# Optimization experiments

Hardware: AMD Instinct MI355X
Metric: run time of the kernel (lower is better)

The kernel has to match this reference:

```python
import jax, jax.numpy as jnp
import numpy as np

B, F, E = 1024, 1024, 256      # batch, flat_shape (mobilenet), embedding_size
L1, L2, L3 = 16, 8, 32         # level1 classes, level2 classes per branch, level3 classes per leaf
NE3 = L1 * L2                  # 128 leaf (level-3) classifier heads


def setup_inputs() -> dict:
    key = jax.random.key(0)
    ks = jax.random.split(key, 10)
    w = lambda k, shape: (jax.random.normal(k, shape, jnp.float32) * 0.02)
    return {
        "features_x": jax.random.normal(ks[0], (B, F), jnp.float32),
        "features_y": jax.random.normal(ks[1], (B, F), jnp.float32),
        # level-1 head: Linear(F->E, no bias) + LayerNorm + ReLU + Linear(E->L1)
        "l1_W1": w(ks[2], (F, E)),
        "l1_g": jnp.ones((E,), jnp.float32), "l1_b": jnp.zeros((E,), jnp.float32),
        "l1_W2": w(ks[3], (E, L1)), "l1_b2": jnp.zeros((L1,), jnp.float32),
        # level-2 heads (one per level-1 class), stacked on a leading expert axis
        "l2_W1": w(ks[4], (L1, F, E)),
        "l2_g": jnp.ones((L1, E), jnp.float32), "l2_b": jnp.zeros((L1, E), jnp.float32),
        "l2_W2": w(ks[5], (L1, E, L2)), "l2_b2": jnp.zeros((L1, L2), jnp.float32),
        # level-3 heads (flattened [level1][level2] -> NE3 experts)
        "l3_W1": w(ks[6], (NE3, F, E)),
        "l3_g": jnp.ones((NE3, E), jnp.float32), "l3_b": jnp.zeros((NE3, E), jnp.float32),
        "l3_W2": w(ks[7], (NE3, E, L3)), "l3_b2": jnp.zeros((NE3, L3), jnp.float32),
    }


def _ln(h, g, b, eps=1e-5):
    m = jnp.mean(h, axis=-1, keepdims=True)
    v = jnp.mean(jnp.square(h - m), axis=-1, keepdims=True)
    return (h - m) * jax.lax.rsqrt(v + eps) * g + b


def reference(features_x, features_y,
              l1_W1, l1_g, l1_b, l1_W2, l1_b2,
              l2_W1, l2_g, l2_b, l2_W2, l2_b2,
              l3_W1, l3_g, l3_b, l3_W2, l3_b2):
    # Dropout is identity in eval mode.
    x, y = features_x, features_y
    rows = jnp.arange(x.shape[0])

    # level 1: single head on x
    h1 = jax.nn.relu(_ln(x @ l1_W1, l1_g, l1_b))
    logits1 = h1 @ l1_W2 + l1_b2                                # [B, L1]
    idx1 = jnp.argmax(logits1, axis=-1)                         # argmax(softmax) == argmax

    # level 2: routed head on 0.6*x + 0.4*y; compute all L1 heads batched, gather selected
    ft = 0.6 * x + 0.4 * y
    h2 = jax.nn.relu(_ln(jnp.einsum('bf,efh->beh', ft, l2_W1), l2_g, l2_b))  # [B, L1, E]
    logits2_all = jnp.einsum('beh,ehc->bec', h2, l2_W2) + l2_b2              # [B, L1, L2]
    logits2 = logits2_all[rows, idx1]                                        # [B, L2]
    idx2 = jnp.argmax(logits2, axis=-1)

    # level 3: doubly-routed head on x; flat expert index = idx1*L2 + idx2
    eidx = idx1 * logits2.shape[-1] + idx2
    h3 = jax.nn.relu(_ln(jnp.einsum('bf,efh->beh', x, l3_W1), l3_g, l3_b))   # [B, NE3, E]
    logits3_all = jnp.einsum('beh,ehc->bec', h3, l3_W2) + l3_b2              # [B, NE3, L3]
    logits3 = logits3_all[rows, eidx]                                        # [B, L3]

    # uniform class counts => pad_sequence is a no-op
    return (logits1, logits2, logits3)
```

## Files before the change

kernel.cpp:

```cpp
#include <hip/hip_runtime.h>


#define B_    1024
#define F_    1024
#define E_    256
#define NL1   16
#define NL2   8
#define NL3   32
#define NE3_  128
#define CS1   2
#define CS2   4
#define CS3   16
#define KS3   4
#define MAXCH2 272
#define MAXCH3 192
#define OUT2_OFF (B_ * NL1)
#define OUT3_OFF (B_ * (NL1 + NL2))
#define H4_BYTE_OFF 65536
#define H4_BYTES   ((size_t)MAXCH3 * KS3 * 16 * E_ * 4)
#define HNS (E_ + 4)

typedef __attribute__((ext_vector_type(8))) short bf16x8_t;
typedef __attribute__((ext_vector_type(4))) float f32x4_t;

__device__ __forceinline__ float b2f(unsigned short u) {
    union { unsigned int i; float f; } v; v.i = ((unsigned int)u) << 16; return v.f;
}
__device__ __forceinline__ unsigned short f2b(float f) {
    union { float f; unsigned int i; } v; v.f = f;
    unsigned int x = v.i; x += 0x7fffu + ((x >> 16) & 1u);
    return (unsigned short)(x >> 16);
}

template<int R, int NC>
__device__ void head_chunk(
    const float* __restrict__ in,
    const void* W1v, const void* gv_, const void* bv_,
    const void* W2v, const void* b2v, int bf,
    float* part, float* hn, float* red, float* lg, int t)
{
    const int lane = t & 63;
    const int grp  = t >> 6;
    const int e0   = lane * 4;

    float acc[R][4];
    #pragma unroll
    for (int r = 0; r < R; ++r) { acc[r][0]=0.f; acc[r][1]=0.f; acc[r][2]=0.f; acc[r][3]=0.f; }

    const float* ing = in + grp * 256;

    if (bf) {
        const unsigned short* W = (const unsigned short*)W1v + (size_t)grp * 256 * E_;
        for (int f0 = 0; f0 < 256; f0 += 16) {
            ushort4 w[16];
            #pragma unroll
            for (int k = 0; k < 16; ++k)
                w[k] = *(const ushort4*)(W + (size_t)(f0 + k) * E_ + e0);
            #pragma unroll
            for (int q = 0; q < 4; ++q) {
                float4 xq[R];
                #pragma unroll
                for (int r = 0; r < R; ++r)
                    xq[r] = *(const float4*)(ing + r * F_ + f0 + q * 4);
                #pragma unroll
                for (int k2 = 0; k2 < 4; ++k2) {
                    ushort4 ww = w[q * 4 + k2];
                    float w0 = b2f(ww.x), w1 = b2f(ww.y), w2 = b2f(ww.z), w3 = b2f(ww.w);
                    #pragma unroll
                    for (int r = 0; r < R; ++r) {
                        float xv = (k2 == 0) ? xq[r].x : (k2 == 1) ? xq[r].y
                                 : (k2 == 2) ? xq[r].z : xq[r].w;
                        acc[r][0] += xv * w0; acc[r][1] += xv * w1;
                        acc[r][2] += xv * w2; acc[r][3] += xv * w3;
                    }
                }
            }
        }
    } else {
        const float* W = (const float*)W1v + (size_t)grp * 256 * E_;
        for (int f0 = 0; f0 < 256; f0 += 8) {
            float4 w[8];
            #pragma unroll
            for (int k = 0; k < 8; ++k)
                w[k] = *(const float4*)(W + (size_t)(f0 + k) * E_ + e0);
            #pragma unroll
            for (int q = 0; q < 2; ++q) {
                float4 xq[R];
                #pragma unroll
                for (int r = 0; r < R; ++r)
                    xq[r] = *(const float4*)(ing + r * F_ + f0 + q * 4);
                #pragma unroll
                for (int k2 = 0; k2 < 4; ++k2) {
                    float4 ww = w[q * 4 + k2];
                    #pragma unroll
                    for (int r = 0; r < R; ++r) {
                        float xv = (k2 == 0) ? xq[r].x : (k2 == 1) ? xq[r].y
                                 : (k2 == 2) ? xq[r].z : xq[r].w;
                        acc[r][0] += xv * ww.x; acc[r][1] += xv * ww.y;
                        acc[r][2] += xv * ww.z; acc[r][3] += xv * ww.w;
                    }
                }
            }
        }
    }

    #pragma unroll
    for (int r = 0; r < R; ++r) {
        part[(size_t)(grp * R + r) * E_ + e0 + 0] = acc[r][0];
        part[(size_t)(grp * R + r) * E_ + e0 + 1] = acc[r][1];
        part[(size_t)(grp * R + r) * E_ + e0 + 2] = acc[r][2];
        part[(size_t)(grp * R + r) * E_ + e0 + 3] = acc[r][3];
    }
    __syncthreads();

    float h[R];
    #pragma unroll
    for (int r = 0; r < R; ++r)
        h[r] = part[(0 * R + r) * E_ + t] + part[(1 * R + r) * E_ + t]
             + part[(2 * R + r) * E_ + t] + part[(3 * R + r) * E_ + t];

    #pragma unroll
    for (int r = 0; r < R; ++r) {
        float s = h[r], ss = h[r] * h[r];
        #pragma unroll
        for (int o = 32; o > 0; o >>= 1) { s += __shfl_xor(s, o); ss += __shfl_xor(ss, o); }
        if (lane == 0) { red[(grp * R + r) * 2 + 0] = s; red[(grp * R + r) * 2 + 1] = ss; }
    }
    __syncthreads();

    float gv, bv;
    if (bf) { gv = b2f(((const unsigned short*)gv_)[t]); bv = b2f(((const unsigned short*)bv_)[t]); }
    else    { gv = ((const float*)gv_)[t];               bv = ((const float*)bv_)[t]; }

    #pragma unroll
    for (int r = 0; r < R; ++r) {
        float S  = red[(0*R+r)*2] + red[(1*R+r)*2] + red[(2*R+r)*2] + red[(3*R+r)*2];
        float SS = red[(0*R+r)*2+1] + red[(1*R+r)*2+1] + red[(2*R+r)*2+1] + red[(3*R+r)*2+1];
        float m    = S * (1.0f / E_);
        float var  = SS * (1.0f / E_) - m * m;
        float rstd = rsqrtf(var + 1e-5f);
        hn[r * HNS + t] = fmaxf((h[r] - m) * rstd * gv + bv, 0.0f);
    }
    __syncthreads();

    constexpr int RN = R * NC;
    constexpr int G  = 4;
    constexpr int CH = E_ / G;
    float a = 0.f;
    if (t < RN * G) {
        const int oi = t % RN, j = t / RN, r = oi / NC, c = oi % NC;
        if (bf) {
            const unsigned short* W = (const unsigned short*)W2v;
            #pragma unroll 8
            for (int e = j * CH; e < j * CH + CH; ++e) a += hn[r * HNS + e] * b2f(W[(size_t)e * NC + c]);
        } else {
            const float* W = (const float*)W2v;
            #pragma unroll 8
            for (int e = j * CH; e < j * CH + CH; ++e) a += hn[r * HNS + e] * W[(size_t)e * NC + c];
        }
    }
    part[t] = a;
    __syncthreads();
    if (t < RN) {
        const int c = t % NC;
        float sum = part[t] + part[RN + t] + part[2 * RN + t] + part[3 * RN + t];
        float bias = bf ? b2f(((const unsigned short*)b2v)[c]) : ((const float*)b2v)[c];
        lg[t] = sum + bias;
    }
    __syncthreads();
}

__global__ void dtype_sniff_kernel(const unsigned int* l1g_words, int* flag) {
    if (threadIdx.x == 0 && blockIdx.x == 0)
        *flag = (l1g_words[0] == 0x3F803F80u) ? 1 : 0;
}

__global__ __launch_bounds__(256) void mlc_level1_kernel(
    const void* x, const void* W1, const void* g, const void* b,
    const void* W2, const void* b2, void* out, int* idx1, const int* flagp)
{
    __shared__ float in_s[CS1 * F_];
    __shared__ float part[4 * CS1 * E_];
    __shared__ float hn[CS1 * HNS];
    __shared__ float red[4 * CS1 * 2];
    __shared__ float lg[CS1 * NL1];

    const int t = threadIdx.x;
    const int bf = *flagp;
    const int row0 = blockIdx.x * CS1;

    #pragma unroll
    for (int r = 0; r < CS1; ++r) {
        if (bf) {
            ushort4 xv = ((const ushort4*)x)[(size_t)(row0 + r) * 256 + t];
            in_s[r * F_ + t*4+0] = b2f(xv.x); in_s[r * F_ + t*4+1] = b2f(xv.y);
            in_s[r * F_ + t*4+2] = b2f(xv.z); in_s[r * F_ + t*4+3] = b2f(xv.w);
        } else {
            float4 xv = ((const float4*)x)[(size_t)(row0 + r) * 256 + t];
            in_s[r * F_ + t*4+0] = xv.x; in_s[r * F_ + t*4+1] = xv.y;
            in_s[r * F_ + t*4+2] = xv.z; in_s[r * F_ + t*4+3] = xv.w;
        }
    }
    __syncthreads();

    head_chunk<CS1, NL1>(in_s, W1, g, b, W2, b2, bf, part, hn, red, lg, t);

    if (t < CS1 * NL1) {
        int r = t / NL1, c = t % NL1;
        size_t o = (size_t)(row0 + r) * NL1 + c;
        if (bf) ((unsigned short*)out)[o] = f2b(lg[t]);
        else    ((float*)out)[o] = lg[t];
        if (c == 0) {
            float best = lg[r * NL1]; int bi = 0;
            #pragma unroll
            for (int cc = 1; cc < NL1; ++cc)
                if (lg[r * NL1 + cc] > best) { best = lg[r * NL1 + cc]; bi = cc; }
            idx1[row0 + r] = bi;
        }
    }
}

template<int NEXP, int MAXCH, int CHUNK>
__global__ __launch_bounds__(1024) void mlc_route_kernel(
    const int* __restrict__ src, int* __restrict__ rows_out, int4* __restrict__ chunks_out)
{
    __shared__ int hist[NEXP], offs[NEXP], cur[NEXP], cOff[NEXP];
    __shared__ int sA[NEXP], sB[NEXP];
    const int t = threadIdx.x;
    if (t < NEXP) hist[t] = 0;
    __syncthreads();
    int e = src[t];
    if (e < 0) e = 0; if (e >= NEXP) e = NEXP - 1;
    atomicAdd(&hist[e], 1);
    __syncthreads();
    if (t < NEXP) { sA[t] = hist[t]; sB[t] = (hist[t] + CHUNK - 1) / CHUNK; }
    __syncthreads();
    for (int d = 1; d < NEXP; d <<= 1) {
        int va = 0, vb = 0;
        if (t < NEXP && t >= d) { va = sA[t - d]; vb = sB[t - d]; }
        __syncthreads();
        if (t < NEXP) { sA[t] += va; sB[t] += vb; }
        __syncthreads();
    }
    if (t < NEXP) {
        int ex = sA[t] - hist[t];
        offs[t] = ex; cur[t] = ex;
        cOff[t] = sB[t] - (hist[t] + CHUNK - 1) / CHUNK;
    }
    __syncthreads();
    int pos = atomicAdd(&cur[e], 1);
    if (pos >= 0 && pos < B_) rows_out[pos] = t;
    const int ctot = sB[NEXP - 1];
    if (t < NEXP) {
        int n = hist[t], st = offs[t], c0 = cOff[t], k = 0;
        for (int j = 0; j < n; j += CHUNK, ++k)
            chunks_out[c0 + k] = make_int4(t, st + j, min(CHUNK, n - j), 0);
    }
    for (int s = ctot + t; s < MAXCH; s += 1024) chunks_out[s] = make_int4(0, 0, 0, 0);
}

__global__ __launch_bounds__(256) void mlc_level2_kernel(
    const void* x, const void* y,
    const void* W1b, const void* gb, const void* bb,
    const void* W2b, const void* b2b,
    const int4* __restrict__ chunks, const int* __restrict__ rowlist,
    void* out, int* eidx, const int* flagp)
{
    __shared__ float in_s[CS2 * F_];
    __shared__ float part[4 * CS2 * E_];
    __shared__ float hn[CS2 * HNS];
    __shared__ float red[4 * CS2 * 2];
    __shared__ float lg[CS2 * NL2];
    __shared__ int4  chs;
    __shared__ int   rows_s[CS2];

    const int t = threadIdx.x;
    const int bf = *flagp;

    if (t == 0) chs = chunks[blockIdx.x];
    __syncthreads();
    const int expert = chs.x, start = chs.y, count = chs.z;
    if (count <= 0) return;
    if (t < CS2) rows_s[t] = (t < count) ? rowlist[start + t] : -1;
    __syncthreads();

    #pragma unroll
    for (int r = 0; r < CS2; ++r) {
        int row = rows_s[r];
        float f0 = 0.f, f1 = 0.f, f2 = 0.f, f3 = 0.f;
        if (row >= 0) {
            if (bf) {
                ushort4 xv = ((const ushort4*)x)[(size_t)row * 256 + t];
                ushort4 yv = ((const ushort4*)y)[(size_t)row * 256 + t];
                f0 = 0.6f * b2f(xv.x) + 0.4f * b2f(yv.x);
                f1 = 0.6f * b2f(xv.y) + 0.4f * b2f(yv.y);
                f2 = 0.6f * b2f(xv.z) + 0.4f * b2f(yv.z);
                f3 = 0.6f * b2f(xv.w) + 0.4f * b2f(yv.w);
            } else {
                float4 xv = ((const float4*)x)[(size_t)row * 256 + t];
                float4 yv = ((const float4*)y)[(size_t)row * 256 + t];
                f0 = 0.6f * xv.x + 0.4f * yv.x; f1 = 0.6f * xv.y + 0.4f * yv.y;
                f2 = 0.6f * xv.z + 0.4f * yv.z; f3 = 0.6f * xv.w + 0.4f * yv.w;
            }
        }
        in_s[r * F_ + t*4+0] = f0; in_s[r * F_ + t*4+1] = f1;
        in_s[r * F_ + t*4+2] = f2; in_s[r * F_ + t*4+3] = f3;
    }
    __syncthreads();

    const void* W1 = bf ? (const void*)((const unsigned short*)W1b + (size_t)expert * F_ * E_)
                        : (const void*)((const float*)W1b + (size_t)expert * F_ * E_);
    const void* g  = bf ? (const void*)((const unsigned short*)gb + (size_t)expert * E_)
                        : (const void*)((const float*)gb + (size_t)expert * E_);
    const void* b  = bf ? (const void*)((const unsigned short*)bb + (size_t)expert * E_)
                        : (const void*)((const float*)bb + (size_t)expert * E_);
    const void* W2 = bf ? (const void*)((const unsigned short*)W2b + (size_t)expert * E_ * NL2)
                        : (const void*)((const float*)W2b + (size_t)expert * E_ * NL2);
    const void* b2 = bf ? (const void*)((const unsigned short*)b2b + (size_t)expert * NL2)
                        : (const void*)((const float*)b2b + (size_t)expert * NL2);

    head_chunk<CS2, NL2>(in_s, W1, g, b, W2, b2, bf, part, hn, red, lg, t);

    if (t < CS2 * NL2) {
        int r = t / NL2, c = t % NL2;
        if (r < count) {
            size_t o = (size_t)OUT2_OFF + (size_t)rows_s[r] * NL2 + c;
            if (bf) ((unsigned short*)out)[o] = f2b(lg[t]);
            else    ((float*)out)[o] = lg[t];
            if (c == 0) {
                float best = lg[r * NL2]; int bi = 0;
                #pragma unroll
                for (int cc = 1; cc < NL2; ++cc)
                    if (lg[r * NL2 + cc] > best) { best = lg[r * NL2 + cc]; bi = cc; }
                eidx[rows_s[r]] = expert * NL2 + bi;
            }
        }
    }
}


__global__ __launch_bounds__(256) void mlc_l3_partial_kernel(
    const void* x, const void* W1b,
    const int4* __restrict__ chunks, const int* __restrict__ rowlist,
    float* __restrict__ h4, const int* flagp)
{
    __shared__ __align__(16) unsigned short xs[16 * 256];
    __shared__ int4 chs;
    __shared__ int  rows_s[16];

    const int t  = threadIdx.x;
    const int bf = *flagp;
    const int c  = blockIdx.x >> 2;
    const int ks = blockIdx.x & 3;

    if (t == 0) chs = chunks[c];
    __syncthreads();
    const int expert = chs.x, start = chs.y, count = chs.z;
    if (count <= 0) return;
    if (t < 16) rows_s[t] = (t < count) ? rowlist[start + t] : -1;
    __syncthreads();

    {
        const int r = t >> 4;
        const int row = rows_s[r];
        #pragma unroll
        for (int i = 0; i < 2; ++i) {
            const int c2 = (t & 15) + 16 * i;
            const int cs = c2 ^ (r & 7);
            uint4 v = make_uint4(0u, 0u, 0u, 0u);
            if (row >= 0) {
                if (bf) {
                    v = *(const uint4*)((const unsigned short*)x + (size_t)row * F_ + ks * 256 + c2 * 8);
                } else {
                    const float* xf = (const float*)x + (size_t)row * F_ + ks * 256 + c2 * 8;
                    float4 fa = *(const float4*)xf;
                    float4 fb = *(const float4*)(xf + 4);
                    v.x = ((unsigned)f2b(fa.y) << 16) | f2b(fa.x);
                    v.y = ((unsigned)f2b(fa.w) << 16) | f2b(fa.z);
                    v.z = ((unsigned)f2b(fb.y) << 16) | f2b(fb.x);
                    v.w = ((unsigned)f2b(fb.w) << 16) | f2b(fb.z);
                }
            }
            *(uint4*)(xs + r * 256 + cs * 8) = v;
        }
    }
    __syncthreads();

    const int l    = t & 63;
    const int w    = t >> 6;
    const int u    = l >> 4;
    const int row  = l & 15;
    const int colb = w * 64 + row;

    f32x4_t acc[4];
    #pragma unroll
    for (int tl = 0; tl < 4; ++tl) acc[tl] = (f32x4_t){0.f, 0.f, 0.f, 0.f};

    if (bf) {
        const unsigned short* __restrict__ W =
            (const unsigned short*)W1b + (size_t)expert * F_ * E_ + (size_t)ks * 256 * E_;
        #pragma unroll 2
        for (int k0 = 0; k0 < 256; k0 += 32) {
            const int cs = ((k0 >> 3) + u) ^ (row & 7);
            bf16x8_t ax = *(const bf16x8_t*)(xs + row * 256 + cs * 8);
            const unsigned short* __restrict__ Wk = W + (size_t)(k0 + u * 8) * E_ + colb;
            #pragma unroll
            for (int tl = 0; tl < 4; ++tl) {
                bf16x8_t b;
                #pragma unroll
                for (int e = 0; e < 8; ++e) b[e] = (short)Wk[e * E_ + tl * 16];
                acc[tl] = __builtin_amdgcn_mfma_f32_16x16x32_bf16(ax, b, acc[tl], 0, 0, 0);
            }
        }
    } else {
        const float* __restrict__ W =
            (const float*)W1b + (size_t)expert * F_ * E_ + (size_t)ks * 256 * E_;
        #pragma unroll 2
        for (int k0 = 0; k0 < 256; k0 += 32) {
            const int cs = ((k0 >> 3) + u) ^ (row & 7);
            bf16x8_t ax = *(const bf16x8_t*)(xs + row * 256 + cs * 8);
            const float* __restrict__ Wk = W + (size_t)(k0 + u * 8) * E_ + colb;
            #pragma unroll
            for (int tl = 0; tl < 4; ++tl) {
                bf16x8_t b;
                #pragma unroll
                for (int e = 0; e < 8; ++e) b[e] = (short)f2b(Wk[e * E_ + tl * 16]);
                acc[tl] = __builtin_amdgcn_mfma_f32_16x16x32_bf16(ax, b, acc[tl], 0, 0, 0);
            }
        }
    }

    float* hd = h4 + (size_t)(c * KS3 + ks) * 16 * E_;
    #pragma unroll
    for (int tl = 0; tl < 4; ++tl) {
        #pragma unroll
        for (int j = 0; j < 4; ++j)
            hd[(size_t)(u * 4 + j) * E_ + colb + tl * 16] = acc[tl][j];
    }
}

__global__ __launch_bounds__(256) void MultiLevelClassifier_26491358282059_kernel(
    const void* gb, const void* bb, const void* W2b, const void* b2b,
    const int4* __restrict__ chunks, const int* __restrict__ rowlist,
    const float* __restrict__ h4, void* out, const int* flagp)
{
    __shared__ float hn[8 * HNS];
    __shared__ float red[4 * 8 * 2];
    __shared__ int4  chs;
    __shared__ int   rows_s[16];

    const int t    = threadIdx.x;
    const int bf   = *flagp;
    const int c    = blockIdx.x >> 1;
    const int half = blockIdx.x & 1;

    if (t == 0) chs = chunks[c];
    __syncthreads();
    const int expert = chs.x, start = chs.y, count = chs.z;
    if (count <= 0) return;
    if (t < 16) rows_s[t] = (t < count) ? rowlist[start + t] : -1;
    __syncthreads();

    const int l = t & 63, w = t >> 6;

    float hv[8];
    #pragma unroll
    for (int m = 0; m < 8; ++m) {
        const float* p = h4 + (size_t)(c * KS3) * 16 * E_ + (size_t)(half * 8 + m) * E_ + t;
        hv[m] = p[0] + p[16 * E_] + p[32 * E_] + p[48 * E_];
    }

    #pragma unroll
    for (int m = 0; m < 8; ++m) {
        float s = hv[m], ss = hv[m] * hv[m];
        #pragma unroll
        for (int o = 32; o > 0; o >>= 1) { s += __shfl_xor(s, o); ss += __shfl_xor(ss, o); }
        if (l == 0) { red[(w * 8 + m) * 2] = s; red[(w * 8 + m) * 2 + 1] = ss; }
    }
    __syncthreads();

    float gv, bv;
    if (bf) {
        gv = b2f(((const unsigned short*)gb)[(size_t)expert * E_ + t]);
        bv = b2f(((const unsigned short*)bb)[(size_t)expert * E_ + t]);
    } else {
        gv = ((const float*)gb)[(size_t)expert * E_ + t];
        bv = ((const float*)bb)[(size_t)expert * E_ + t];
    }

    #pragma unroll
    for (int m = 0; m < 8; ++m) {
        float S  = red[m * 2]     + red[(8 + m) * 2]     + red[(16 + m) * 2]     + red[(24 + m) * 2];
        float SS = red[m * 2 + 1] + red[(8 + m) * 2 + 1] + red[(16 + m) * 2 + 1] + red[(24 + m) * 2 + 1];
        float mean = S * (1.0f / E_);
        float var  = SS * (1.0f / E_) - mean * mean;
        float rstd = rsqrtf(var + 1e-5f);
        hn[m * HNS + t] = fmaxf((hv[m] - mean) * rstd * gv + bv, 0.0f);
    }
    __syncthreads();

    {
        const int r = t >> 5, c0 = t & 31;
        float a = 0.f;
        if (bf) {
            const unsigned short* W = (const unsigned short*)W2b + (size_t)expert * E_ * NL3;
            #pragma unroll 8
            for (int e = 0; e < E_; ++e) a += hn[r * HNS + e] * b2f(W[(size_t)e * NL3 + c0]);
        } else {
            const float* W = (const float*)W2b + (size_t)expert * E_ * NL3;
            #pragma unroll 8
            for (int e = 0; e < E_; ++e) a += hn[r * HNS + e] * W[(size_t)e * NL3 + c0];
        }
        const int rr = half * 8 + r;
        if (rr < count) {
            float bias = bf ? b2f(((const unsigned short*)b2b)[(size_t)expert * NL3 + c0])
                            : ((const float*)b2b)[(size_t)expert * NL3 + c0];
            size_t o = (size_t)OUT3_OFF + (size_t)rows_s[rr] * NL3 + c0;
            if (bf) ((unsigned short*)out)[o] = f2b(a + bias);
            else    ((float*)out)[o] = a + bias;
        }
    }
}

__device__ __forceinline__ void stage_rows_full(
    unsigned short* xs, const void* xg, const int* rows, int bf, int t)
{
    const int r = t >> 4;
    const int row = rows[r];
    #pragma unroll
    for (int i = 0; i < 8; ++i) {
        const int c  = (t & 15) + 16 * i;
        const int cs = c ^ (r & 7);
        uint4 v = make_uint4(0u, 0u, 0u, 0u);
        if (row >= 0) {
            if (bf) {
                v = *(const uint4*)((const unsigned short*)xg + (size_t)row * F_ + c * 8);
            } else {
                const float* xf = (const float*)xg + (size_t)row * F_ + c * 8;
                float4 fa = *(const float4*)xf;
                float4 fb = *(const float4*)(xf + 4);
                v.x = ((unsigned)f2b(fa.y) << 16) | f2b(fa.x);
                v.y = ((unsigned)f2b(fa.w) << 16) | f2b(fa.z);
                v.z = ((unsigned)f2b(fb.y) << 16) | f2b(fb.x);
                v.w = ((unsigned)f2b(fb.w) << 16) | f2b(fb.z);
            }
        }
        *(uint4*)(xs + (size_t)r * F_ + cs * 8) = v;
    }
}

__global__ __launch_bounds__(256) void mlc_level3_mono_kernel(
    const void* x,
    const void* W1b, const void* gb, const void* bb,
    const void* W2b, const void* b2b,
    const int4* __restrict__ chunks, const int* __restrict__ rowlist,
    void* out, const int* flagp)
{
    __shared__ __align__(16) unsigned short xs[16 * F_];
    __shared__ float h[16 * E_];
    __shared__ float red[128];
    __shared__ int4  chs;
    __shared__ int   rows_s[16];

    const int t  = threadIdx.x;
    const int bf = *flagp;

    if (t == 0) chs = chunks[blockIdx.x];
    __syncthreads();
    const int expert = chs.x, start = chs.y, count = chs.z;
    if (count <= 0) return;
    if (t < 16) rows_s[t] = (t < count) ? rowlist[start + t] : -1;
    __syncthreads();

    stage_rows_full(xs, x, rows_s, bf, t);
    __syncthreads();

    const int l = t & 63, w = t >> 6, u = l >> 4, row = l & 15;
    const int colb = w * 64 + row;
    f32x4_t acc[4];
    #pragma unroll
    for (int tl = 0; tl < 4; ++tl) acc[tl] = (f32x4_t){0.f, 0.f, 0.f, 0.f};

    if (bf) {
        const unsigned short* __restrict__ W = (const unsigned short*)W1b + (size_t)expert * F_ * E_;
        for (int k0 = 0; k0 < F_; k0 += 32) {
            const int cs = ((k0 >> 3) + u) ^ (row & 7);
            bf16x8_t ax = *(const bf16x8_t*)(xs + (size_t)row * F_ + cs * 8);
            const unsigned short* __restrict__ Wk = W + (size_t)(k0 + u * 8) * E_ + colb;
            #pragma unroll
            for (int tl = 0; tl < 4; ++tl) {
                bf16x8_t b;
                #pragma unroll
                for (int e = 0; e < 8; ++e) b[e] = (short)Wk[e * E_ + tl * 16];
                acc[tl] = __builtin_amdgcn_mfma_f32_16x16x32_bf16(ax, b, acc[tl], 0, 0, 0);
            }
        }
    } else {
        const float* __restrict__ W = (const float*)W1b + (size_t)expert * F_ * E_;
        for (int k0 = 0; k0 < F_; k0 += 32) {
            const int cs = ((k0 >> 3) + u) ^ (row & 7);
            bf16x8_t ax = *(const bf16x8_t*)(xs + (size_t)row * F_ + cs * 8);
            const float* __restrict__ Wk = W + (size_t)(k0 + u * 8) * E_ + colb;
            #pragma unroll
            for (int tl = 0; tl < 4; ++tl) {
                bf16x8_t b;
                #pragma unroll
                for (int e = 0; e < 8; ++e) b[e] = (short)f2b(Wk[e * E_ + tl * 16]);
                acc[tl] = __builtin_amdgcn_mfma_f32_16x16x32_bf16(ax, b, acc[tl], 0, 0, 0);
            }
        }
    }
    #pragma unroll
    for (int tl = 0; tl < 4; ++tl) {
        #pragma unroll
        for (int j = 0; j < 4; ++j)
            h[(size_t)(u * 4 + j) * E_ + colb + tl * 16] = acc[tl][j];
    }
    __syncthreads();

    float hv[16];
    #pragma unroll
    for (int r = 0; r < 16; ++r) hv[r] = h[(size_t)r * E_ + t];
    #pragma unroll
    for (int r = 0; r < 16; ++r) {
        float s = hv[r], ss = hv[r] * hv[r];
        #pragma unroll
        for (int o = 32; o > 0; o >>= 1) { s += __shfl_xor(s, o); ss += __shfl_xor(ss, o); }
        if (l == 0) { red[(w * 16 + r) * 2] = s; red[(w * 16 + r) * 2 + 1] = ss; }
    }
    __syncthreads();
    float gv, bv;
    if (bf) { gv = b2f(((const unsigned short*)gb)[(size_t)expert * E_ + t]);
              bv = b2f(((const unsigned short*)bb)[(size_t)expert * E_ + t]); }
    else    { gv = ((const float*)gb)[(size_t)expert * E_ + t];
              bv = ((const float*)bb)[(size_t)expert * E_ + t]; }
    #pragma unroll
    for (int r = 0; r < 16; ++r) {
        float S  = red[r * 2]     + red[(16 + r) * 2]     + red[(32 + r) * 2]     + red[(48 + r) * 2];
        float SS = red[r * 2 + 1] + red[(16 + r) * 2 + 1] + red[(32 + r) * 2 + 1] + red[(48 + r) * 2 + 1];
        float mean = S * (1.0f / E_);
        float var  = SS * (1.0f / E_) - mean * mean;
        float rstd = rsqrtf(var + 1e-5f);
        h[(size_t)r * E_ + t] = fmaxf((hv[r] - mean) * rstd * gv + bv, 0.0f);
    }
    __syncthreads();

    {
        const int r = t >> 4, c0 = t & 15;
        float a0 = 0.f, a1 = 0.f;
        if (bf) {
            const unsigned short* W = (const unsigned short*)W2b + (size_t)expert * E_ * NL3;
            #pragma unroll 4
            for (int e = 0; e < E_; ++e) {
                float hh = h[(size_t)r * E_ + e];
                a0 += hh * b2f(W[(size_t)e * NL3 + c0]);
                a1 += hh * b2f(W[(size_t)e * NL3 + c0 + 16]);
            }
        } else {
            const float* W = (const float*)W2b + (size_t)expert * E_ * NL3;
            #pragma unroll 4
            for (int e = 0; e < E_; ++e) {
                float hh = h[(size_t)r * E_ + e];
                a0 += hh * W[(size_t)e * NL3 + c0];
                a1 += hh * W[(size_t)e * NL3 + c0 + 16];
            }
        }
        if (r < count) {
            float bb0, bb1;
            if (bf) { bb0 = b2f(((const unsigned short*)b2b)[(size_t)expert * NL3 + c0]);
                      bb1 = b2f(((const unsigned short*)b2b)[(size_t)expert * NL3 + c0 + 16]); }
            else    { bb0 = ((const float*)b2b)[(size_t)expert * NL3 + c0];
                      bb1 = ((const float*)b2b)[(size_t)expert * NL3 + c0 + 16]; }
            size_t o = (size_t)OUT3_OFF + (size_t)rows_s[r] * NL3 + c0;
            if (bf) {
                ((unsigned short*)out)[o]      = f2b(a0 + bb0);
                ((unsigned short*)out)[o + 16] = f2b(a1 + bb1);
            } else {
                ((float*)out)[o]      = a0 + bb0;
                ((float*)out)[o + 16] = a1 + bb1;
            }
        }
    }
}

extern "C" void kernel_launch(void* const* d_in, const int* in_sizes, int n_in,
                              void* d_out, int out_size, void* d_ws, size_t ws_size,
                              hipStream_t stream) {
    (void)in_sizes; (void)n_in; (void)out_size;

    int* ws = (int*)d_ws;
    int*  flag  = ws;
    int*  idx1  = ws + 64;
    int*  eidx  = ws + 1088;
    int*  rows2 = ws + 2112;
    int*  rows3 = ws + 3136;
    int4* ch2   = (int4*)(ws + 4160);
    int4* ch3   = (int4*)(ws + 5248);
    float* h4   = (float*)((char*)d_ws + H4_BYTE_OFF);

    const bool big_ws = ws_size >= (size_t)H4_BYTE_OFF + H4_BYTES;

    dtype_sniff_kernel<<<1, 1, 0, stream>>>((const unsigned int*)d_in[3], flag);

    mlc_level1_kernel<<<B_ / CS1, 256, 0, stream>>>(
        d_in[0], d_in[2], d_in[3], d_in[4], d_in[5], d_in[6],
        d_out, idx1, flag);

    mlc_route_kernel<NL1, MAXCH2, CS2><<<1, 1024, 0, stream>>>(idx1, rows2, ch2);

    mlc_level2_kernel<<<MAXCH2, 256, 0, stream>>>(
        d_in[0], d_in[1], d_in[7], d_in[8], d_in[9], d_in[10], d_in[11],
        ch2, rows2, d_out, eidx, flag);

    mlc_route_kernel<NE3_, MAXCH3, CS3><<<1, 1024, 0, stream>>>(eidx, rows3, ch3);

    if (big_ws) {
        mlc_l3_partial_kernel<<<MAXCH3 * KS3, 256, 0, stream>>>(
            d_in[0], d_in[12], ch3, rows3, h4, flag);
        MultiLevelClassifier_26491358282059_kernel<<<MAXCH3 * 2, 256, 0, stream>>>(
            d_in[13], d_in[14], d_in[15], d_in[16],
            ch3, rows3, h4, d_out, flag);
    } else {
        mlc_level3_mono_kernel<<<MAXCH3, 256, 0, stream>>>(
            d_in[0], d_in[12], d_in[13], d_in[14], d_in[15], d_in[16],
            ch3, rows3, d_out, flag);
    }
}
```

Before: 329.1 us.

## Move level-1 and level-2 heads to split-K bf16 MFMA with near-tie fp32 cleanup

After: 516.5 us. 57.0% more time.

```diff
diff --git a/kernel.cpp b/kernel.cpp
--- a/kernel.cpp
+++ b/kernel.cpp
@@ -8,17 +8,18 @@
 #define NL2   8
 #define NL3   32
 #define NE3_  128
-#define CS1   2
-#define CS2   4
-#define CS3   16
-#define KS3   4
-#define MAXCH2 272
+#define NCH1  64
+#define MAXCH2 80
 #define MAXCH3 192
 #define OUT2_OFF (B_ * NL1)
 #define OUT3_OFF (B_ * (NL1 + NL2))
 #define H4_BYTE_OFF 65536
-#define H4_BYTES   ((size_t)MAXCH3 * KS3 * 16 * E_ * 4)
+#define H4_BYTES   ((size_t)MAXCH3 * 4 * 16 * E_ * 4)
 #define HNS (E_ + 4)
+#define MARGIN 4.0e-3f
+#define CS1F  2
+#define CS2F  4
+#define MAXCH2F 272
 
 typedef __attribute__((ext_vector_type(8))) short bf16x8_t;
 typedef __attribute__((ext_vector_type(4))) float f32x4_t;
@@ -170,27 +171,581 @@
     __syncthreads();
 }
 
-__global__ void dtype_sniff_kernel(const unsigned int* l1g_words, int* flag) {
-    if (threadIdx.x == 0 && blockIdx.x == 0)
+__global__ void dtype_sniff_kernel(const unsigned int* l1g_words, int* flag,
+                                   int* fcnt1, int* fcnt2) {
+    if (threadIdx.x == 0 && blockIdx.x == 0) {
         *flag = (l1g_words[0] == 0x3F803F80u) ? 1 : 0;
-}
-
-__global__ __launch_bounds__(256) void mlc_level1_kernel(
+        *fcnt1 = 0; *fcnt2 = 0;
+    }
+}
+
+template<int DUAL>
+__device__ __forceinline__ void mfma_slice(
+    const unsigned short* xs, const unsigned short* ys,
+    const void* Wv, int bf, f32x4_t accx[4], f32x4_t accy[4], int t)
+{
+    const int l = t & 63, w = t >> 6, u = l >> 4, row = l & 15;
+    const int colb = w * 64 + row;
+    if (bf) {
+        const unsigned short* __restrict__ W = (const unsigned short*)Wv;
+        #pragma unroll 2
+        for (int k0 = 0; k0 < 256; k0 += 32) {
+            const int cs = ((k0 >> 3) + u) ^ (row & 7);
+            bf16x8_t ax = *(const bf16x8_t*)(xs + row * 256 + cs * 8);
+            bf16x8_t ay{};
+            if (DUAL) ay = *(const bf16x8_t*)(ys + row * 256 + cs * 8);
+            const unsigned short* __restrict__ Wk = W + (size_t)(k0 + u * 8) * E_ + colb;
+            #pragma unroll
+            for (int tl = 0; tl < 4; ++tl) {
+                bf16x8_t b;
+                #pragma unroll
+                for (int e = 0; e < 8; ++e) b[e] = (short)Wk[e * E_ + tl * 16];
+                accx[tl] = __builtin_amdgcn_mfma_f32_16x16x32_bf16(ax, b, accx[tl], 0, 0, 0);
+                if (DUAL)
+                    accy[tl] = __builtin_amdgcn_mfma_f32_16x16x32_bf16(ay, b, accy[tl], 0, 0, 0);
+            }
+        }
+    } else {
+        const float* __restrict__ W = (const float*)Wv;
+        #pragma unroll 2
+        for (int k0 = 0; k0 < 256; k0 += 32) {
+            const int cs = ((k0 >> 3) + u) ^ (row & 7);
+            bf16x8_t ax = *(const bf16x8_t*)(xs + row * 256 + cs * 8);
+            bf16x8_t ay{};
+            if (DUAL) ay = *(const bf16x8_t*)(ys + row * 256 + cs * 8);
+            const float* __restrict__ Wk = W + (size_t)(k0 + u * 8) * E_ + colb;
+            #pragma unroll
+            for (int tl = 0; tl < 4; ++tl) {
+                bf16x8_t b;
+                #pragma unroll
+                for (int e = 0; e < 8; ++e) b[e] = (short)f2b(Wk[e * E_ + tl * 16]);
+                accx[tl] = __builtin_amdgcn_mfma_f32_16x16x32_bf16(ax, b, accx[tl], 0, 0, 0);
+                if (DUAL)
+                    accy[tl] = __builtin_amdgcn_mfma_f32_16x16x32_bf16(ay, b, accy[tl], 0, 0, 0);
+            }
+        }
+    }
+}
+
+__device__ __forceinline__ void stage_slice_row(
+    unsigned short* xs, const void* xg, int row, int ks, int bf, int t)
+{
+    const int r = t >> 4;
+    #pragma unroll
+    for (int i = 0; i < 2; ++i) {
+        const int c2 = (t & 15) + 16 * i;
+        const int cs = c2 ^ (r & 7);
+        uint4 v = make_uint4(0u, 0u, 0u, 0u);
+        if (row >= 0) {
+            if (bf) {
+                v = *(const uint4*)((const unsigned short*)xg + (size_t)row * F_ + ks * 256 + c2 * 8);
+            } else {
+                const float* xf = (const float*)xg + (size_t)row * F_ + ks * 256 + c2 * 8;
+                float4 fa = *(const float4*)xf;
+                float4 fb = *(const float4*)(xf + 4);
+                v.x = ((unsigned)f2b(fa.y) << 16) | f2b(fa.x);
+                v.y = ((unsigned)f2b(fa.w) << 16) | f2b(fa.z);
+                v.z = ((unsigned)f2b(fb.y) << 16) | f2b(fb.x);
+                v.w = ((unsigned)f2b(fb.w) << 16) | f2b(fb.z);
+            }
+        }
+        *(uint4*)(xs + r * 256 + cs * 8) = v;
+    }
+}
+
+__device__ __forceinline__ void write_slice(float* hd, const f32x4_t acc[4], int t) {
+    const int l = t & 63, w = t >> 6, u = l >> 4, row = l & 15;
+    const int colb = w * 64 + row;
+    #pragma unroll
+    for (int tl = 0; tl < 4; ++tl) {
+        #pragma unroll
+        for (int j = 0; j < 4; ++j)
+            hd[(size_t)(u * 4 + j) * E_ + colb + tl * 16] = acc[tl][j];
+    }
+}
+
+__global__ __launch_bounds__(256) void mlc_l1_partial_kernel(
+    const void* x, const void* W1, float* __restrict__ h4, const int* flagp)
+{
+    __shared__ __align__(16) unsigned short xs[16 * 256];
+    const int t = threadIdx.x, bf = *flagp;
+    const int c = blockIdx.x >> 2, ks = blockIdx.x & 3;
+    stage_slice_row(xs, x, c * 16 + (t >> 4), ks, bf, t);
+    __syncthreads();
+    f32x4_t acc[4];
+    #pragma unroll
+    for (int tl = 0; tl < 4; ++tl) acc[tl] = (f32x4_t){0.f, 0.f, 0.f, 0.f};
+    const void* Ws = bf ? (const void*)((const unsigned short*)W1 + (size_t)ks * 256 * E_)
+                        : (const void*)((const float*)W1 + (size_t)ks * 256 * E_);
+    mfma_slice<0>(xs, nullptr, Ws, bf, acc, nullptr, t);
+    write_slice(h4 + (size_t)(c * 4 + ks) * 16 * E_, acc, t);
+}
+
+__global__ __launch_bounds__(256) void mlc_l1_final_kernel(
+    const void* g, const void* b, const void* W2, const void* b2,
+    const float* __restrict__ h4, void* out, int* idx1,
+    int* fcnt, int* flist, const int* flagp)
+{
+    __shared__ float hn[8 * HNS];
+    __shared__ float red[64];
+    __shared__ float lgs[8 * NL1];
+    const int t = threadIdx.x, bf = *flagp;
+    const int c = blockIdx.x >> 1, half = blockIdx.x & 1;
+    const int l = t & 63, w = t >> 6;
+
+    float hv[8];
+    #pragma unroll
+    for (int m = 0; m < 8; ++m) {
+        const float* p = h4 + (size_t)(c * 4) * 16 * E_ + (size_t)(half * 8 + m) * E_ + t;
+        hv[m] = p[0] + p[16 * E_] + p[32 * E_] + p[48 * E_];
+    }
+    #pragma unroll
+    for (int m = 0; m < 8; ++m) {
+        float s = hv[m], ss = hv[m] * hv[m];
+        #pragma unroll
+        for (int o = 32; o > 0; o >>= 1) { s += __shfl_xor(s, o); ss += __shfl_xor(ss, o); }
+        if (l == 0) { red[(w * 8 + m) * 2] = s; red[(w * 8 + m) * 2 + 1] = ss; }
+    }
+    __syncthreads();
+    float gv, bv;
+    if (bf) { gv = b2f(((const unsigned short*)g)[t]); bv = b2f(((const unsigned short*)b)[t]); }
+    else    { gv = ((const float*)g)[t];               bv = ((const float*)b)[t]; }
+    #pragma unroll
+    for (int m = 0; m < 8; ++m) {
+        float S  = red[m * 2]     + red[(8 + m) * 2]     + red[(16 + m) * 2]     + red[(24 + m) * 2];
+        float SS = red[m * 2 + 1] + red[(8 + m) * 2 + 1] + red[(16 + m) * 2 + 1] + red[(24 + m) * 2 + 1];
+        float mean = S * (1.0f / E_);
+        float var  = SS * (1.0f / E_) - mean * mean;
+        float rstd = rsqrtf(var + 1e-5f);
+        hn[m * HNS + t] = fmaxf((hv[m] - mean) * rstd * gv + bv, 0.0f);
+    }
+    __syncthreads();
+
+    if (t < 128) {
+        const int r = t >> 4, c0 = t & 15;
+        float a = 0.f;
+        if (bf) {
+            const unsigned short* W = (const unsigned short*)W2;
+            #pragma unroll 8
+            for (int e = 0; e < E_; ++e) a += hn[r * HNS + e] * b2f(W[(size_t)e * NL1 + c0]);
+        } else {
+            const float* W = (const float*)W2;
+            #pragma unroll 8
+            for (int e = 0; e < E_; ++e) a += hn[r * HNS + e] * W[(size_t)e * NL1 + c0];
+        }
+        float bias = bf ? b2f(((const unsigned short*)b2)[c0]) : ((const float*)b2)[c0];
+        lgs[r * NL1 + c0] = a + bias;
+    }
+    __syncthreads();
+
+    if (t < 128) {
+        const int r = t >> 4, c0 = t & 15;
+        const int row = c * 16 + half * 8 + r;
+        size_t o = (size_t)row * NL1 + c0;
+        if (bf) ((unsigned short*)out)[o] = f2b(lgs[r * NL1 + c0]);
+        else    ((float*)out)[o] = lgs[r * NL1 + c0];
+    }
+    if (t < 8) {
+        const int row = c * 16 + half * 8 + t;
+        float best = lgs[t * NL1]; int bi = 0; float sec = -3.4e38f;
+        #pragma unroll
+        for (int cc = 1; cc < NL1; ++cc) {
+            float v = lgs[t * NL1 + cc];
+            if (v > best) { sec = best; best = v; bi = cc; }
+            else if (v > sec) sec = v;
+        }
+        idx1[row] = bi;
+        if (best - sec < MARGIN) { int p = atomicAdd(fcnt, 1); flist[p] = row; }
+    }
+}
+
+__global__ __launch_bounds__(256) void mlc_l1_cleanup_kernel(
+    const void* x, const void* W1, const void* g, const void* b,
+    const void* W2, const void* b2, void* out, int* idx1,
+    const int* fcnt, const int* flist, const int* flagp)
+{
+    __shared__ float in_s[F_];
+    __shared__ float part[4 * E_];
+    __shared__ float hn[HNS];
+    __shared__ float red[8];
+    __shared__ float lg[NL1];
+    const int t = threadIdx.x, bf = *flagp;
+    const int n = *fcnt;
+    for (int i = blockIdx.x; i < n; i += gridDim.x) {
+        const int row = flist[i];
+        if (bf) {
+            ushort4 xv = ((const ushort4*)x)[(size_t)row * 256 + t];
+            in_s[t*4+0] = b2f(xv.x); in_s[t*4+1] = b2f(xv.y);
+            in_s[t*4+2] = b2f(xv.z); in_s[t*4+3] = b2f(xv.w);
+        } else {
+            float4 xv = ((const float4*)x)[(size_t)row * 256 + t];
+            in_s[t*4+0] = xv.x; in_s[t*4+1] = xv.y; in_s[t*4+2] = xv.z; in_s[t*4+3] = xv.w;
+        }
+        __syncthreads();
+        head_chunk<1, NL1>(in_s, W1, g, b, W2, b2, bf, part, hn, red, lg, t);
+        if (t < NL1) {
+            size_t o = (size_t)row * NL1 + t;
+            if (bf) ((unsigned short*)out)[o] = f2b(lg[t]);
+            else    ((float*)out)[o] = lg[t];
+        }
+        if (t == 0) {
+            float best = lg[0]; int bi = 0;
+            #pragma unroll
+            for (int cc = 1; cc < NL1; ++cc)
+                if (lg[cc] > best) { best = lg[cc]; bi = cc; }
+            idx1[row] = bi;
+        }
+        __syncthreads();
+    }
+}
+
+template<int NEXP, int MAXCH, int CHUNK>
+__global__ __launch_bounds__(1024) void mlc_route_kernel(
+    const int* __restrict__ src, int* __restrict__ rows_out, int4* __restrict__ chunks_out)
+{
+    __shared__ int hist[NEXP], offs[NEXP], cur[NEXP], cOff[NEXP];
+    __shared__ int sA[NEXP], sB[NEXP];
+    const int t = threadIdx.x;
+    if (t < NEXP) hist[t] = 0;
+    __syncthreads();
+    int e = src[t];
+    if (e < 0) e = 0; if (e >= NEXP) e = NEXP - 1;
+    atomicAdd(&hist[e], 1);
+    __syncthreads();
+    if (t < NEXP) { sA[t] = hist[t]; sB[t] = (hist[t] + CHUNK - 1) / CHUNK; }
+    __syncthreads();
+    for (int d = 1; d < NEXP; d <<= 1) {
+        int va = 0, vb = 0;
+        if (t < NEXP && t >= d) { va = sA[t - d]; vb = sB[t - d]; }
+        __syncthreads();
+        if (t < NEXP) { sA[t] += va; sB[t] += vb; }
+        __syncthreads();
+    }
+    if (t < NEXP) {
+        int ex = sA[t] - hist[t];
+        offs[t] = ex; cur[t] = ex;
+        cOff[t] = sB[t] - (hist[t] + CHUNK - 1) / CHUNK;
+    }
+    __syncthreads();
+    int pos = atomicAdd(&cur[e], 1);
+    if (pos >= 0 && pos < B_) rows_out[pos] = t;
+    const int ctot = sB[NEXP - 1];
+    if (t < NEXP) {
+        int n = hist[t], st = offs[t], c0 = cOff[t], k = 0;
+        for (int j = 0; j < n; j += CHUNK, ++k)
+            chunks_out[c0 + k] = make_int4(t, st + j, min(CHUNK, n - j), 0);
+    }
+    for (int s = ctot + t; s < MAXCH; s += 1024) chunks_out[s] = make_int4(0, 0, 0, 0);
+}
+
+__global__ __launch_bounds__(256) void mlc_l2_partial_kernel(
+    const void* x, const void* y, const void* W1b,
+    const int4* __restrict__ chunks, const int* __restrict__ rowlist,
+    float* __restrict__ h4, const int* flagp)
+{
+    __shared__ __align__(16) unsigned short xs[16 * 256];
+    __shared__ __align__(16) unsigned short ys[16 * 256];
+    __shared__ int4 chs;
+    __shared__ int  rows_s[16];
+    const int t = threadIdx.x, bf = *flagp;
+    const int c = blockIdx.x >> 2, ks = blockIdx.x & 3;
+
+    if (t == 0) chs = chunks[c];
+    __syncthreads();
+    const int expert = chs.x, start = chs.y, count = chs.z;
+    if (count <= 0) return;
+    if (t < 16) rows_s[t] = (t < count) ? rowlist[start + t] : -1;
+    __syncthreads();
+
+    stage_slice_row(xs, x, rows_s[t >> 4], ks, bf, t);
+    stage_slice_row(ys, y, rows_s[t >> 4], ks, bf, t);
+    __syncthreads();
+
+    f32x4_t ax[4], ay[4];
+    #pragma unroll
+    for (int tl = 0; tl < 4; ++tl) { ax[tl] = (f32x4_t){0.f,0.f,0.f,0.f}; ay[tl] = (f32x4_t){0.f,0.f,0.f,0.f}; }
+    const void* Ws = bf ? (const void*)((const unsigned short*)W1b + (size_t)expert * F_ * E_ + (size_t)ks * 256 * E_)
+                        : (const void*)((const float*)W1b + (size_t)expert * F_ * E_ + (size_t)ks * 256 * E_);
+    mfma_slice<1>(xs, ys, Ws, bf, ax, ay, t);
+    #pragma unroll
+    for (int tl = 0; tl < 4; ++tl)
+        #pragma unroll
+        for (int j = 0; j < 4; ++j) ax[tl][j] = 0.6f * ax[tl][j] + 0.4f * ay[tl][j];
+    write_slice(h4 + (size_t)(c * 4 + ks) * 16 * E_, ax, t);
+}
+
+__global__ __launch_bounds__(256) void mlc_l2_final_kernel(
+    const void* gb, const void* bb, const void* W2b, const void* b2b,
+    const int4* __restrict__ chunks, const int* __restrict__ rowlist,
+    const float* __restrict__ h4, void* out, int* eidx,
+    int* fcnt, int* flist, const int* flagp)
+{
+    __shared__ float hn[8 * HNS];
+    __shared__ float red[64];
+    __shared__ float lgs[8 * NL2];
+    __shared__ int4  chs;
+    __shared__ int   rows_s[16];
+    const int t = threadIdx.x, bf = *flagp;
+    const int c = blockIdx.x >> 1, half = blockIdx.x & 1;
+
+    if (t == 0) chs = chunks[c];
+    __syncthreads();
+    const int expert = chs.x, start = chs.y, count = chs.z;
+    if (count <= 0) return;
+    if (t < 16) rows_s[t] = (t < count) ? rowlist[start + t] : -1;
+    __syncthreads();
+    const int l = t & 63, w = t >> 6;
+
+    float hv[8];
+    #pragma unroll
+    for (int m = 0; m < 8; ++m) {
+        const float* p = h4 + (size_t)(c * 4) * 16 * E_ + (size_t)(half * 8 + m) * E_ + t;
+        hv[m] = p[0] + p[16 * E_] + p[32 * E_] + p[48 * E_];
+    }
+    #pragma unroll
+    for (int m = 0; m < 8; ++m) {
+        float s = hv[m], ss = hv[m] * hv[m];
+        #pragma unroll
+        for (int o = 32; o > 0; o >>= 1) { s += __shfl_xor(s, o); ss += __shfl_xor(ss, o); }
+        if (l == 0) { red[(w * 8 + m) * 2] = s; red[(w * 8 + m) * 2 + 1] = ss; }
+    }
+    __syncthreads();
+    float gv, bv;
+    if (bf) { gv = b2f(((const unsigned short*)gb)[(size_t)expert * E_ + t]);
+              bv = b2f(((const unsigned short*)bb)[(size_t)expert * E_ + t]); }
+    else    { gv = ((const float*)gb)[(size_t)expert * E_ + t];
+              bv = ((const float*)bb)[(size_t)expert * E_ + t]; }
+    #pragma unroll
+    for (int m = 0; m < 8; ++m) {
+        float S  = red[m * 2]     + red[(8 + m) * 2]     + red[(16 + m) * 2]     + red[(24 + m) * 2];
+        float SS = red[m * 2 + 1] + red[(8 + m) * 2 + 1] + red[(16 + m) * 2 + 1] + red[(24 + m) * 2 + 1];
+        float mean = S * (1.0f / E_);
+        float var  = SS * (1.0f / E_) - mean * mean;
+        float rstd = rsqrtf(var + 1e-5f);
+        hn[m * HNS + t] = fmaxf((hv[m] - mean) * rstd * gv + bv, 0.0f);
+    }
+    __syncthreads();
+
+    if (t < 64) {
+        const int r = t >> 3, c0 = t & 7;
+        float a = 0.f;
+        if (bf) {
+            const unsigned short* W = (const unsigned short*)W2b + (size_t)expert * E_ * NL2;
+            #pragma unroll 8
+            for (int e = 0; e < E_; ++e) a += hn[r * HNS + e] * b2f(W[(size_t)e * NL2 + c0]);
+        } else {
+            const float* W = (const float*)W2b + (size_t)expert * E_ * NL2;
+            #pragma unroll 8
+            for (int e = 0; e < E_; ++e) a += hn[r * HNS + e] * W[(size_t)e * NL2 + c0];
+        }
+        float bias = bf ? b2f(((const unsigned short*)b2b)[(size_t)expert * NL2 + c0])
+                        : ((const float*)b2b)[(size_t)expert * NL2 + c0];
+        lgs[r * NL2 + c0] = a + bias;
+    }
+    __syncthreads();
+
+    if (t < 64) {
+        const int r = t >> 3, c0 = t & 7;
+        const int rr = half * 8 + r;
+        if (rr < count) {
+            size_t o = (size_t)OUT2_OFF + (size_t)rows_s[rr] * NL2 + c0;
+            if (bf) ((unsigned short*)out)[o] = f2b(lgs[r * NL2 + c0]);
+            else    ((float*)out)[o] = lgs[r * NL2 + c0];
+        }
+    }
+    if (t < 8) {
+        const int rr = half * 8 + t;
+        if (rr < count) {
+            const int row = rows_s[rr];
+            float best = lgs[t * NL2]; int bi = 0; float sec = -3.4e38f;
+            #pragma unroll
+            for (int cc = 1; cc < NL2; ++cc) {
+                float v = lgs[t * NL2 + cc];
+                if (v > best) { sec = best; best = v; bi = cc; }
+                else if (v > sec) sec = v;
+            }
+            eidx[row] = expert * NL2 + bi;
+            if (best - sec < MARGIN) { int p = atomicAdd(fcnt, 1); flist[p] = row; }
+        }
+    }
+}
+
+__global__ __launch_bounds__(256) void mlc_l2_cleanup_kernel(
+    const void* x, const void* y,
+    const void* W1b, const void* gb, const void* bb,
+    const void* W2b, const void* b2b,
+    void* out, int* eidx, const int* idx1,
+    const int* fcnt, const int* flist, const int* flagp)
+{
+    __shared__ float in_s[F_];
+    __shared__ float part[4 * E_];
+    __shared__ float hn[HNS];
+    __shared__ float red[8];
+    __shared__ float lg[NL2];
+    const int t = threadIdx.x, bf = *flagp;
+    const int n = *fcnt;
+    for (int i = blockIdx.x; i < n; i += gridDim.x) {
+        const int row = flist[i];
+        const int expert = idx1[row];
+        if (bf) {
+            ushort4 xv = ((const ushort4*)x)[(size_t)row * 256 + t];
+            ushort4 yv = ((const ushort4*)y)[(size_t)row * 256 + t];
+            in_s[t*4+0] = 0.6f * b2f(xv.x) + 0.4f * b2f(yv.x);
+            in_s[t*4+1] = 0.6f * b2f(xv.y) + 0.4f * b2f(yv.y);
+            in_s[t*4+2] = 0.6f * b2f(xv.z) + 0.4f * b2f(yv.z);
+            in_s[t*4+3] = 0.6f * b2f(xv.w) + 0.4f * b2f(yv.w);
+        } else {
+            float4 xv = ((const float4*)x)[(size_t)row * 256 + t];
+            float4 yv = ((const float4*)y)[(size_t)row * 256 + t];
+            in_s[t*4+0] = 0.6f * xv.x + 0.4f * yv.x;
+            in_s[t*4+1] = 0.6f * xv.y + 0.4f * yv.y;
+            in_s[t*4+2] = 0.6f * xv.z + 0.4f * yv.z;
+            in_s[t*4+3] = 0.6f * xv.w + 0.4f * yv.w;
+        }
+        __syncthreads();
+        const void* W1 = bf ? (const void*)((const unsigned short*)W1b + (size_t)expert * F_ * E_)
+                            : (const void*)((const float*)W1b + (size_t)expert * F_ * E_);
+        const void* g  = bf ? (const void*)((const unsigned short*)gb + (size_t)expert * E_)
+                            : (const void*)((const float*)gb + (size_t)expert * E_);
+        const void* b  = bf ? (const void*)((const unsigned short*)bb + (size_t)expert * E_)
+                            : (const void*)((const float*)bb + (size_t)expert * E_);
+        const void* W2 = bf ? (const void*)((const unsigned short*)W2b + (size_t)expert * E_ * NL2)
+                            : (const void*)((const float*)W2b + (size_t)expert * E_ * NL2);
+        const void* b2 = bf ? (const void*)((const unsigned short*)b2b + (size_t)expert * NL2)
+                            : (const void*)((const float*)b2b + (size_t)expert * NL2);
+        head_chunk<1, NL2>(in_s, W1, g, b, W2, b2, bf, part, hn, red, lg, t);
+        if (t < NL2) {
+            size_t o = (size_t)OUT2_OFF + (size_t)row * NL2 + t;
+            if (bf) ((unsigned short*)out)[o] = f2b(lg[t]);
+            else    ((float*)out)[o] = lg[t];
+        }
+        if (t == 0) {
+            float best = lg[0]; int bi = 0;
+            #pragma unroll
+            for (int cc = 1; cc < NL2; ++cc)
+                if (lg[cc] > best) { best = lg[cc]; bi = cc; }
+            eidx[row] = expert * NL2 + bi;
+        }
+        __syncthreads();
+    }
+}
+
+__global__ __launch_bounds__(256) void mlc_l3_partial_kernel(
+    const void* x, const void* W1b,
+    const int4* __restrict__ chunks, const int* __restrict__ rowlist,
+    float* __restrict__ h4, const int* flagp)
+{
+    __shared__ __align__(16) unsigned short xs[16 * 256];
+    __shared__ int4 chs;
+    __shared__ int  rows_s[16];
+    const int t = threadIdx.x, bf = *flagp;
+    const int c = blockIdx.x >> 2, ks = blockIdx.x & 3;
+
+    if (t == 0) chs = chunks[c];
+    __syncthreads();
+    const int expert = chs.x, start = chs.y, count = chs.z;
+    if (count <= 0) return;
+    if (t < 16) rows_s[t] = (t < count) ? rowlist[start + t] : -1;
+    __syncthreads();
+
+    stage_slice_row(xs, x, rows_s[t >> 4], ks, bf, t);
+    __syncthreads();
+
+    f32x4_t acc[4];
+    #pragma unroll
+    for (int tl = 0; tl < 4; ++tl) acc[tl] = (f32x4_t){0.f, 0.f, 0.f, 0.f};
+    const void* Ws = bf ? (const void*)((const unsigned short*)W1b + (size_t)expert * F_ * E_ + (size_t)ks * 256 * E_)
+                        : (const void*)((const float*)W1b + (size_t)expert * F_ * E_ + (size_t)ks * 256 * E_);
+    mfma_slice<0>(xs, nullptr, Ws, bf, acc, nullptr, t);
+    write_slice(h4 + (size_t)(c * 4 + ks) * 16 * E_, acc, t);
+}
+
+__global__ __launch_bounds__(256) void MultiLevelClassifier_26491358282059_kernel(
+    const void* gb, const void* bb, const void* W2b, const void* b2b,
+    const int4* __restrict__ chunks, const int* __restrict__ rowlist,
+    const float* __restrict__ h4, void* out, const int* flagp)
+{
+    __shared__ float hn[8 * HNS];
+    __shared__ float red[64];
+    __shared__ int4  chs;
+    __shared__ int   rows_s[16];
+    const int t = threadIdx.x, bf = *flagp;
+    const int c = blockIdx.x >> 1, half = blockIdx.x & 1;
+
+    if (t == 0) chs = chunks[c];
+    __syncthreads();
+    const int expert = chs.x, start = chs.y, count = chs.z;
+    if (count <= 0) return;
+    if (t < 16) rows_s[t] = (t < count) ? rowlist[start + t] : -1;
+    __syncthreads();
+    const int l = t & 63, w = t >> 6;
+
+    float hv[8];
+    #pragma unroll
+    for (int m = 0; m < 8; ++m) {
+        const float* p = h4 + (size_t)(c * 4) * 16 * E_ + (size_t)(half * 8 + m) * E_ + t;
+        hv[m] = p[0] + p[16 * E_] + p[32 * E_] + p[48 * E_];
+    }
+    #pragma unroll
+    for (int m = 0; m < 8; ++m) {
+        float s = hv[m], ss = hv[m] * hv[m];
+        #pragma unroll
+        for (int o = 32; o > 0; o >>= 1) { s += __shfl_xor(s, o); ss += __shfl_xor(ss, o); }
+        if (l == 0) { red[(w * 8 + m) * 2] = s; red[(w * 8 + m) * 2 + 1] = ss; }
+    }
+    __syncthreads();
+    float gv, bv;
+    if (bf) { gv = b2f(((const unsigned short*)gb)[(size_t)expert * E_ + t]);
+              bv = b2f(((const unsigned short*)bb)[(size_t)expert * E_ + t]); }
+    else    { gv = ((const float*)gb)[(size_t)expert * E_ + t];
+              bv = ((const float*)bb)[(size_t)expert * E_ + t]; }
+    #pragma unroll
+    for (int m = 0; m < 8; ++m) {
+        float S  = red[m * 2]     + red[(8 + m) * 2]     + red[(16 + m) * 2]     + red[(24 + m) * 2];
+        float SS = red[m * 2 + 1] + red[(8 + m) * 2 + 1] + red[(16 + m) * 2 + 1] + red[(24 + m) * 2 + 1];
+        float mean = S * (1.0f / E_);
+        float var  = SS * (1.0f / E_) - mean * mean;
+        float rstd = rsqrtf(var + 1e-5f);
+        hn[m * HNS + t] = fmaxf((hv[m] - mean) * rstd * gv + bv, 0.0f);
+    }
+    __syncthreads();
+
+    {
+        const int r = t >> 5, c0 = t & 31;
+        float a = 0.f;
+        if (bf) {
+            const unsigned short* W = (const unsigned short*)W2b + (size_t)expert * E_ * NL3;
+            #pragma unroll 8
+            for (int e = 0; e < E_; ++e) a += hn[r * HNS + e] * b2f(W[(size_t)e * NL3 + c0]);
+        } else {
+            const float* W = (const float*)W2b + (size_t)expert * E_ * NL3;
+            #pragma unroll 8
+            for (int e = 0; e < E_; ++e) a += hn[r * HNS + e] * W[(size_t)e * NL3 + c0];
+        }
+        const int rr = half * 8 + r;
+        if (rr < count) {
+            float bias = bf ? b2f(((const unsigned short*)b2b)[(size_t)expert * NL3 + c0])
+                            : ((const float*)b2b)[(size_t)expert * NL3 + c0];
+            size_t o = (size_t)OUT3_OFF + (size_t)rows_s[rr] * NL3 + c0;
+            if (bf) ((unsigned short*)out)[o] = f2b(a + bias);
+            else    ((float*)out)[o] = a + bias;
+        }
+    }
+}
+
+__global__ __launch_bounds__(256) void mlc_level1_scalar_kernel(
     const void* x, const void* W1, const void* g, const void* b,
     const void* W2, const void* b2, void* out, int* idx1, const int* flagp)
 {
-    __shared__ float in_s[CS1 * F_];
-    __shared__ float part[4 * CS1 * E_];
-    __shared__ float hn[CS1 * HNS];
-    __shared__ float red[4 * CS1 * 2];
-    __shared__ float lg[CS1 * NL1];
-
-    const int t = threadIdx.x;
-    const int bf = *flagp;
-    const int row0 = blockIdx.x * CS1;
-
-    #pragma unroll
-    for (int r = 0; r < CS1; ++r) {
+    __shared__ float in_s[CS1F * F_];
+    __shared__ float part[4 * CS1F * E_];
+    __shared__ float hn[CS1F * HNS];
+    __shared__ float red[4 * CS1F * 2];
+    __shared__ float lg[CS1F * NL1];
+    const int t = threadIdx.x, bf = *flagp;
+    const int row0 = blockIdx.x * CS1F;
+    #pragma unroll
+    for (int r = 0; r < CS1F; ++r) {
         if (bf) {
             ushort4 xv = ((const ushort4*)x)[(size_t)(row0 + r) * 256 + t];
             in_s[r * F_ + t*4+0] = b2f(xv.x); in_s[r * F_ + t*4+1] = b2f(xv.y);
@@ -202,10 +757,8 @@
         }
     }
     __syncthreads();
-
-    head_chunk<CS1, NL1>(in_s, W1, g, b, W2, b2, bf, part, hn, red, lg, t);
-
-    if (t < CS1 * NL1) {
+    head_chunk<CS1F, NL1>(in_s, W1, g, b, W2, b2, bf, part, hn, red, lg, t);
+    if (t < CS1F * NL1) {
         int r = t / NL1, c = t % NL1;
         size_t o = (size_t)(row0 + r) * NL1 + c;
         if (bf) ((unsigned short*)out)[o] = f2b(lg[t]);
@@ -220,72 +773,29 @@
     }
 }
 
-template<int NEXP, int MAXCH, int CHUNK>
-__global__ __launch_bounds__(1024) void mlc_route_kernel(
-    const int* __restrict__ src, int* __restrict__ rows_out, int4* __restrict__ chunks_out)
-{
-    __shared__ int hist[NEXP], offs[NEXP], cur[NEXP], cOff[NEXP];
-    __shared__ int sA[NEXP], sB[NEXP];
-    const int t = threadIdx.x;
-    if (t < NEXP) hist[t] = 0;
-    __syncthreads();
-    int e = src[t];
-    if (e < 0) e = 0; if (e >= NEXP) e = NEXP - 1;
-    atomicAdd(&hist[e], 1);
-    __syncthreads();
-    if (t < NEXP) { sA[t] = hist[t]; sB[t] = (hist[t] + CHUNK - 1) / CHUNK; }
-    __syncthreads();
-    for (int d = 1; d < NEXP; d <<= 1) {
-        int va = 0, vb = 0;
-        if (t < NEXP && t >= d) { va = sA[t - d]; vb = sB[t - d]; }
-        __syncthreads();
-        if (t < NEXP) { sA[t] += va; sB[t] += vb; }
-        __syncthreads();
-    }
-    if (t < NEXP) {
-        int ex = sA[t] - hist[t];
-        offs[t] = ex; cur[t] = ex;
-        cOff[t] = sB[t] - (hist[t] + CHUNK - 1) / CHUNK;
-    }
-    __syncthreads();
-    int pos = atomicAdd(&cur[e], 1);
-    if (pos >= 0 && pos < B_) rows_out[pos] = t;
-    const int ctot = sB[NEXP - 1];
-    if (t < NEXP) {
-        int n = hist[t], st = offs[t], c0 = cOff[t], k = 0;
-        for (int j = 0; j < n; j += CHUNK, ++k)
-            chunks_out[c0 + k] = make_int4(t, st + j, min(CHUNK, n - j), 0);
-    }
-    for (int s = ctot + t; s < MAXCH; s += 1024) chunks_out[s] = make_int4(0, 0, 0, 0);
-}
-
-__global__ __launch_bounds__(256) void mlc_level2_kernel(
+__global__ __launch_bounds__(256) void mlc_level2_scalar_kernel(
     const void* x, const void* y,
     const void* W1b, const void* gb, const void* bb,
     const void* W2b, const void* b2b,
     const int4* __restrict__ chunks, const int* __restrict__ rowlist,
     void* out, int* eidx, const int* flagp)
 {
-    __shared__ float in_s[CS2 * F_];
-    __shared__ float part[4 * CS2 * E_];
-    __shared__ float hn[CS2 * HNS];
-    __shared__ float red[4 * CS2 * 2];
-    __shared__ float lg[CS2 * NL2];
+    __shared__ float in_s[CS2F * F_];
+    __shared__ float part[4 * CS2F * E_];
+    __shared__ float hn[CS2F * HNS];
+    __shared__ float red[4 * CS2F * 2];
+    __shared__ float lg[CS2F * NL2];
     __shared__ int4  chs;
-    __shared__ int   rows_s[CS2];
-
-    const int t = threadIdx.x;
-    const int bf = *flagp;
-
+    __shared__ int   rows_s[CS2F];
+    const int t = threadIdx.x, bf = *flagp;
     if (t == 0) chs = chunks[blockIdx.x];
     __syncthreads();
     const int expert = chs.x, start = chs.y, count = chs.z;
     if (count <= 0) return;
-    if (t < CS2) rows_s[t] = (t < count) ? rowlist[start + t] : -1;
-    __syncthreads();
-
-    #pragma unroll
-    for (int r = 0; r < CS2; ++r) {
+    if (t < CS2F) rows_s[t] = (t < count) ? rowlist[start + t] : -1;
+    __syncthreads();
+    #pragma unroll
+    for (int r = 0; r < CS2F; ++r) {
         int row = rows_s[r];
         float f0 = 0.f, f1 = 0.f, f2 = 0.f, f3 = 0.f;
         if (row >= 0) {
@@ -307,7 +817,6 @@
         in_s[r * F_ + t*4+2] = f2; in_s[r * F_ + t*4+3] = f3;
     }
     __syncthreads();
-
     const void* W1 = bf ? (const void*)((const unsigned short*)W1b + (size_t)expert * F_ * E_)
                         : (const void*)((const float*)W1b + (size_t)expert * F_ * E_);
     const void* g  = bf ? (const void*)((const unsigned short*)gb + (size_t)expert * E_)
@@ -318,10 +827,8 @@
                         : (const void*)((const float*)W2b + (size_t)expert * E_ * NL2);
     const void* b2 = bf ? (const void*)((const unsigned short*)b2b + (size_t)expert * NL2)
                         : (const void*)((const float*)b2b + (size_t)expert * NL2);
-
-    head_chunk<CS2, NL2>(in_s, W1, g, b, W2, b2, bf, part, hn, red, lg, t);
-
-    if (t < CS2 * NL2) {
+    head_chunk<CS2F, NL2>(in_s, W1, g, b, W2, b2, bf, part, hn, red, lg, t);
+    if (t < CS2F * NL2) {
         int r = t / NL2, c = t % NL2;
         if (r < count) {
             size_t o = (size_t)OUT2_OFF + (size_t)rows_s[r] * NL2 + c;
@@ -338,41 +845,37 @@
     }
 }
 
-
-__global__ __launch_bounds__(256) void mlc_l3_partial_kernel(
-    const void* x, const void* W1b,
+__global__ __launch_bounds__(256) void mlc_level3_mono_kernel(
+    const void* x,
+    const void* W1b, const void* gb, const void* bb,
+    const void* W2b, const void* b2b,
     const int4* __restrict__ chunks, const int* __restrict__ rowlist,
-    float* __restrict__ h4, const int* flagp)
-{
-    __shared__ __align__(16) unsigned short xs[16 * 256];
-    __shared__ int4 chs;
-    __shared__ int  rows_s[16];
-
-    const int t  = threadIdx.x;
-    const int bf = *flagp;
-    const int c  = blockIdx.x >> 2;
-    const int ks = blockIdx.x & 3;
-
-    if (t == 0) chs = chunks[c];
+    void* out, const int* flagp)
+{
+    __shared__ __align__(16) unsigned short xs[16 * F_];
+    __shared__ float h[16 * E_];
+    __shared__ float red[128];
+    __shared__ int4  chs;
+    __shared__ int   rows_s[16];
+    const int t = threadIdx.x, bf = *flagp;
+    if (t == 0) chs = chunks[blockIdx.x];
     __syncthreads();
     const int expert = chs.x, start = chs.y, count = chs.z;
     if (count <= 0) return;
     if (t < 16) rows_s[t] = (t < count) ? rowlist[start + t] : -1;
     __syncthreads();
-
     {
         const int r = t >> 4;
         const int row = rows_s[r];
         #pragma unroll
-        for (int i = 0; i < 2; ++i) {
+        for (int i = 0; i < 8; ++i) {
             const int c2 = (t & 15) + 16 * i;
             const int cs = c2 ^ (r & 7);
             uint4 v = make_uint4(0u, 0u, 0u, 0u);
             if (row >= 0) {
-                if (bf) {
-                    v = *(const uint4*)((const unsigned short*)x + (size_t)row * F_ + ks * 256 + c2 * 8);
-                } else {
-                    const float* xf = (const float*)x + (size_t)row * F_ + ks * 256 + c2 * 8;
+                if (bf) v = *(const uint4*)((const unsigned short*)x + (size_t)row * F_ + c2 * 8);
+                else {
+                    const float* xf = (const float*)x + (size_t)row * F_ + c2 * 8;
                     float4 fa = *(const float4*)xf;
                     float4 fb = *(const float4*)(xf + 4);
                     v.x = ((unsigned)f2b(fa.y) << 16) | f2b(fa.x);
@@ -381,206 +884,15 @@
                     v.w = ((unsigned)f2b(fb.w) << 16) | f2b(fb.z);
                 }
             }
-            *(uint4*)(xs + r * 256 + cs * 8) = v;
-        }
-    }
-    __syncthreads();
-
-    const int l    = t & 63;
-    const int w    = t >> 6;
-    const int u    = l >> 4;
-    const int row  = l & 15;
-    const int colb = w * 64 + row;
-
-    f32x4_t acc[4];
-    #pragma unroll
-    for (int tl = 0; tl < 4; ++tl) acc[tl] = (f32x4_t){0.f, 0.f, 0.f, 0.f};
-
-    if (bf) {
-        const unsigned short* __restrict__ W =
-            (const unsigned short*)W1b + (size_t)expert * F_ * E_ + (size_t)ks * 256 * E_;
-        #pragma unroll 2
-        for (int k0 = 0; k0 < 256; k0 += 32) {
-            const int cs = ((k0 >> 3) + u) ^ (row & 7);
-            bf16x8_t ax = *(const bf16x8_t*)(xs + row * 256 + cs * 8);
-            const unsigned short* __restrict__ Wk = W + (size_t)(k0 + u * 8) * E_ + colb;
-            #pragma unroll
-            for (int tl = 0; tl < 4; ++tl) {
-                bf16x8_t b;
-                #pragma unroll
-                for (int e = 0; e < 8; ++e) b[e] = (short)Wk[e * E_ + tl * 16];
-                acc[tl] = __builtin_amdgcn_mfma_f32_16x16x32_bf16(ax, b, acc[tl], 0, 0, 0);
-            }
-        }
-    } else {
-        const float* __restrict__ W =
-            (const float*)W1b + (size_t)expert * F_ * E_ + (size_t)ks * 256 * E_;
-        #pragma unroll 2
-        for (int k0 = 0; k0 < 256; k0 += 32) {
-            const int cs = ((k0 >> 3) + u) ^ (row & 7);
-            bf16x8_t ax = *(const bf16x8_t*)(xs + row * 256 + cs * 8);
-            const float* __restrict__ Wk = W + (size_t)(k0 + u * 8) * E_ + colb;
-            #pragma unroll
-            for (int tl = 0; tl < 4; ++tl) {
-                bf16x8_t b;
-                #pragma unroll
-                for (int e = 0; e < 8; ++e) b[e] = (short)f2b(Wk[e * E_ + tl * 16]);
-                acc[tl] = __builtin_amdgcn_mfma_f32_16x16x32_bf16(ax, b, acc[tl], 0, 0, 0);
-            }
-        }
-    }
-
-    float* hd = h4 + (size_t)(c * KS3 + ks) * 16 * E_;
-    #pragma unroll
-    for (int tl = 0; tl < 4; ++tl) {
-        #pragma unroll
-        for (int j = 0; j < 4; ++j)
-            hd[(size_t)(u * 4 + j) * E_ + colb + tl * 16] = acc[tl][j];
-    }
-}
-
-__global__ __launch_bounds__(256) void MultiLevelClassifier_26491358282059_kernel(
-    const void* gb, const void* bb, const void* W2b, const void* b2b,
-    const int4* __restrict__ chunks, const int* __restrict__ rowlist,
-    const float* __restrict__ h4, void* out, const int* flagp)
-{
-    __shared__ float hn[8 * HNS];
-    __shared__ float red[4 * 8 * 2];
-    __shared__ int4  chs;
-    __shared__ int   rows_s[16];
-
-    const int t    = threadIdx.x;
-    const int bf   = *flagp;
-    const int c    = blockIdx.x >> 1;
-    const int half = blockIdx.x & 1;
-
-    if (t == 0) chs = chunks[c];
-    __syncthreads();
-    const int expert = chs.x, start = chs.y, count = chs.z;
-    if (count <= 0) return;
-    if (t < 16) rows_s[t] = (t < count) ? rowlist[start + t] : -1;
-    __syncthreads();
-
-    const int l = t & 63, w = t >> 6;
-
-    float hv[8];
-    #pragma unroll
-    for (int m = 0; m < 8; ++m) {
-        const float* p = h4 + (size_t)(c * KS3) * 16 * E_ + (size_t)(half * 8 + m) * E_ + t;
-        hv[m] = p[0] + p[16 * E_] + p[32 * E_] + p[48 * E_];
-    }
-
-    #pragma unroll
-    for (int m = 0; m < 8; ++m) {
-        float s = hv[m], ss = hv[m] * hv[m];
-        #pragma unroll
-        for (int o = 32; o > 0; o >>= 1) { s += __shfl_xor(s, o); ss += __shfl_xor(ss, o); }
-        if (l == 0) { red[(w * 8 + m) * 2] = s; red[(w * 8 + m) * 2 + 1] = ss; }
-    }
-    __syncthreads();
-
-    float gv, bv;
-    if (bf) {
-        gv = b2f(((const unsigned short*)gb)[(size_t)expert * E_ + t]);
-        bv = b2f(((const unsigned short*)bb)[(size_t)expert * E_ + t]);
-    } else {
-        gv = ((const float*)gb)[(size_t)expert * E_ + t];
-        bv = ((const float*)bb)[(size_t)expert * E_ + t];
-    }
-
-    #pragma unroll
-    for (int m = 0; m < 8; ++m) {
-        float S  = red[m * 2]     + red[(8 + m) * 2]     + red[(16 + m) * 2]     + red[(24 + m) * 2];
-        float SS = red[m * 2 + 1] + red[(8 + m) * 2 + 1] + red[(16 + m) * 2 + 1] + red[(24 + m) * 2 + 1];
-        float mean = S * (1.0f / E_);
-        float var  = SS * (1.0f / E_) - mean * mean;
-        float rstd = rsqrtf(var + 1e-5f);
-        hn[m * HNS + t] = fmaxf((hv[m] - mean) * rstd * gv + bv, 0.0f);
-    }
-    __syncthreads();
-
-    {
-        const int r = t >> 5, c0 = t & 31;
-        float a = 0.f;
-        if (bf) {
-            const unsigned short* W = (const unsigned short*)W2b + (size_t)expert * E_ * NL3;
-            #pragma unroll 8
-            for (int e = 0; e < E_; ++e) a += hn[r * HNS + e] * b2f(W[(size_t)e * NL3 + c0]);
-        } else {
-            const float* W = (const float*)W2b + (size_t)expert * E_ * NL3;
-            #pragma unroll 8
-            for (int e = 0; e < E_; ++e) a += hn[r * HNS + e] * W[(size_t)e * NL3 + c0];
-        }
-        const int rr = half * 8 + r;
-        if (rr < count) {
-            float bias = bf ? b2f(((const unsigned short*)b2b)[(size_t)expert * NL3 + c0])
-                            : ((const float*)b2b)[(size_t)expert * NL3 + c0];
-            size_t o = (size_t)OUT3_OFF + (size_t)rows_s[rr] * NL3 + c0;
-            if (bf) ((unsigned short*)out)[o] = f2b(a + bias);
-            else    ((float*)out)[o] = a + bias;
-        }
-    }
-}
-
-__device__ __forceinline__ void stage_rows_full(
-    unsigned short* xs, const void* xg, const int* rows, int bf, int t)
-{
-    const int r = t >> 4;
-    const int row = rows[r];
-    #pragma unroll
-    for (int i = 0; i < 8; ++i) {
-        const int c  = (t & 15) + 16 * i;
-        const int cs = c ^ (r & 7);
-        uint4 v = make_uint4(0u, 0u, 0u, 0u);
-        if (row >= 0) {
-            if (bf) {
-                v = *(const uint4*)((const unsigned short*)xg + (size_t)row * F_ + c * 8);
-            } else {
-                const float* xf = (const float*)xg + (size_t)row * F_ + c * 8;
-                float4 fa = *(const float4*)xf;
-                float4 fb = *(const float4*)(xf + 4);
-                v.x = ((unsigned)f2b(fa.y) << 16) | f2b(fa.x);
-                v.y = ((unsigned)f2b(fa.w) << 16) | f2b(fa.z);
-                v.z = ((unsigned)f2b(fb.y) << 16) | f2b(fb.x);
-                v.w = ((unsigned)f2b(fb.w) << 16) | f2b(fb.z);
-            }
-        }
-        *(uint4*)(xs + (size_t)r * F_ + cs * 8) = v;
-    }
-}
-
-__global__ __launch_bounds__(256) void mlc_level3_mono_kernel(
-    const void* x,
-    const void* W1b, const void* gb, const void* bb,
-    const void* W2b, const void* b2b,
-    const int4* __restrict__ chunks, const int* __restrict__ rowlist,
-    void* out, const int* flagp)
-{
-    __shared__ __align__(16) unsigned short xs[16 * F_];
-    __shared__ float h[16 * E_];
-    __shared__ float red[128];
-    __shared__ int4  chs;
-    __shared__ int   rows_s[16];
-
-    const int t  = threadIdx.x;
-    const int bf = *flagp;
-
-    if (t == 0) chs = chunks[blockIdx.x];
-    __syncthreads();
-    const int expert = chs.x, start = chs.y, count = chs.z;
-    if (count <= 0) return;
-    if (t < 16) rows_s[t] = (t < count) ? rowlist[start + t] : -1;
-    __syncthreads();
-
-    stage_rows_full(xs, x, rows_s, bf, t);
-    __syncthreads();
-
+            *(uint4*)(xs + (size_t)r * F_ + cs * 8) = v;
+        }
+    }
+    __syncthreads();
     const int l = t & 63, w = t >> 6, u = l >> 4, row = l & 15;
     const int colb = w * 64 + row;
     f32x4_t acc[4];
     #pragma unroll
     for (int tl = 0; tl < 4; ++tl) acc[tl] = (f32x4_t){0.f, 0.f, 0.f, 0.f};
-
     if (bf) {
         const unsigned short* __restrict__ W = (const unsigned short*)W1b + (size_t)expert * F_ * E_;
         for (int k0 = 0; k0 < F_; k0 += 32) {
@@ -611,13 +923,11 @@
         }
     }
     #pragma unroll
-    for (int tl = 0; tl < 4; ++tl) {
+    for (int tl = 0; tl < 4; ++tl)
         #pragma unroll
         for (int j = 0; j < 4; ++j)
             h[(size_t)(u * 4 + j) * E_ + colb + tl * 16] = acc[tl][j];
-    }
-    __syncthreads();
-
+    __syncthreads();
     float hv[16];
     #pragma unroll
     for (int r = 0; r < 16; ++r) hv[r] = h[(size_t)r * E_ + t];
@@ -644,7 +954,6 @@
         h[(size_t)r * E_ + t] = fmaxf((hv[r] - mean) * rstd * gv + bv, 0.0f);
     }
     __syncthreads();
-
     {
         const int r = t >> 4, c0 = t & 15;
         float a0 = 0.f, a1 = 0.f;
@@ -689,38 +998,56 @@
     (void)in_sizes; (void)n_in; (void)out_size;
 
     int* ws = (int*)d_ws;
-    int*  flag  = ws;
-    int*  idx1  = ws + 64;
-    int*  eidx  = ws + 1088;
-    int*  rows2 = ws + 2112;
-    int*  rows3 = ws + 3136;
-    int4* ch2   = (int4*)(ws + 4160);
-    int4* ch3   = (int4*)(ws + 5248);
-    float* h4   = (float*)((char*)d_ws + H4_BYTE_OFF);
+    int*  flag   = ws;
+    int*  fcnt1  = ws + 1;
+    int*  fcnt2  = ws + 2;
+    int*  idx1   = ws + 64;
+    int*  eidx   = ws + 1088;
+    int*  rows2  = ws + 2112;
+    int*  rows3  = ws + 3136;
+    int*  flist1 = ws + 4160;
+    int*  flist2 = ws + 5184;
+    int4* ch2    = (int4*)(ws + 6208);
+    int4* ch3    = (int4*)(ws + 7296);
+    float* h4    = (float*)((char*)d_ws + H4_BYTE_OFF);
 
     const bool big_ws = ws_size >= (size_t)H4_BYTE_OFF + H4_BYTES;
 
-    dtype_sniff_kernel<<<1, 1, 0, stream>>>((const unsigned int*)d_in[3], flag);
-
-    mlc_level1_kernel<<<B_ / CS1, 256, 0, stream>>>(
-        d_in[0], d_in[2], d_in[3], d_in[4], d_in[5], d_in[6],
-        d_out, idx1, flag);
-
-    mlc_route_kernel<NL1, MAXCH2, CS2><<<1, 1024, 0, stream>>>(idx1, rows2, ch2);
-
-    mlc_level2_kernel<<<MAXCH2, 256, 0, stream>>>(
-        d_in[0], d_in[1], d_in[7], d_in[8], d_in[9], d_in[10], d_in[11],
-        ch2, rows2, d_out, eidx, flag);
-
-    mlc_route_kernel<NE3_, MAXCH3, CS3><<<1, 1024, 0, stream>>>(eidx, rows3, ch3);
+    dtype_sniff_kernel<<<1, 1, 0, stream>>>((const unsigned int*)d_in[3], flag, fcnt1, fcnt2);
 
     if (big_ws) {
-        mlc_l3_partial_kernel<<<MAXCH3 * KS3, 256, 0, stream>>>(
+        mlc_l1_partial_kernel<<<NCH1 * 4, 256, 0, stream>>>(d_in[0], d_in[2], h4, flag);
+        mlc_l1_final_kernel<<<NCH1 * 2, 256, 0, stream>>>(
+            d_in[3], d_in[4], d_in[5], d_in[6], h4, d_out, idx1, fcnt1, flist1, flag);
+        mlc_l1_cleanup_kernel<<<64, 256, 0, stream>>>(
+            d_in[0], d_in[2], d_in[3], d_in[4], d_in[5], d_in[6],
+            d_out, idx1, fcnt1, flist1, flag);
+
+        mlc_route_kernel<NL1, MAXCH2, 16><<<1, 1024, 0, stream>>>(idx1, rows2, ch2);
+
+        mlc_l2_partial_kernel<<<MAXCH2 * 4, 256, 0, stream>>>(
+            d_in[0], d_in[1], d_in[7], ch2, rows2, h4, flag);
+        mlc_l2_final_kernel<<<MAXCH2 * 2, 256, 0, stream>>>(
+            d_in[8], d_in[9], d_in[10], d_in[11], ch2, rows2, h4,
+            d_out, eidx, fcnt2, flist2, flag);
+        mlc_l2_cleanup_kernel<<<64, 256, 0, stream>>>(
+            d_in[0], d_in[1], d_in[7], d_in[8], d_in[9], d_in[10], d_in[11],
+            d_out, eidx, idx1, fcnt2, flist2, flag);
+
+        mlc_route_kernel<NE3_, MAXCH3, 16><<<1, 1024, 0, stream>>>(eidx, rows3, ch3);
+
+        mlc_l3_partial_kernel<<<MAXCH3 * 4, 256, 0, stream>>>(
             d_in[0], d_in[12], ch3, rows3, h4, flag);
         MultiLevelClassifier_26491358282059_kernel<<<MAXCH3 * 2, 256, 0, stream>>>(
-            d_in[13], d_in[14], d_in[15], d_in[16],
-            ch3, rows3, h4, d_out, flag);
+            d_in[13], d_in[14], d_in[15], d_in[16], ch3, rows3, h4, d_out, flag);
     } else {
+        mlc_level1_scalar_kernel<<<B_ / CS1F, 256, 0, stream>>>(
+            d_in[0], d_in[2], d_in[3], d_in[4], d_in[5], d_in[6], d_out, idx1, flag);
+        mlc_route_kernel<NL1, MAXCH2F, CS2F><<<1, 1024, 0, stream>>>(idx1, rows2, ch2);
+        mlc_level2_scalar_kernel<<<MAXCH2F, 256, 0, stream>>>(
+            d_in[0], d_in[1], d_in[7], d_in[8], d_in[9], d_in[10], d_in[11],
+            ch2, rows2, d_out, eidx, flag);
+        mlc_route_kernel<NE3_, MAXCH3, 16><<<1, 1024, 0, stream>>>(eidx, rows3, ch3);
         mlc_level3_mono_kernel<<<MAXCH3, 256, 0, stream>>>(
             d_in[0], d_in[12], d_in[13], d_in[14], d_in[15], d_in[16],
             ch3, rows3, d_out, flag);
```
